# Kernel optimization log

Measured on AMD Instinct MI355X. Metric: run time of the kernel, lower is better.

Reference implementation:

```python
import jax, jax.numpy as jnp
import numpy as np


def squash(s, axis=-1):
    sq = jnp.sum(s * s, axis=axis, keepdims=True)
    return sq / (1.0 + sq) * s / (jnp.sqrt(sq) + 1e-8)


def setup_inputs() -> dict:
    key = jax.random.key(0)
    k1, k2 = jax.random.split(key)
    B, IN_CAPS, IN_DIM = 32, 2048, 16
    NUM_CAPS, CAPS_DIM = 32, 32
    x = jax.random.normal(k1, (B, IN_CAPS, IN_DIM), dtype=jnp.float32)
    W = 0.01 * jax.random.normal(k2, (NUM_CAPS, IN_CAPS, CAPS_DIM, IN_DIM), dtype=jnp.float32)
    return {"x": x, "W": W, "routing_steps": 3}


def reference(x, W, routing_steps):
    # u_hat[b, j, i, c] = W[j, i, c, d] @ x[b, i, d]
    u_hat = jnp.einsum('jicd,bid->bjic', W, x)
    du = jax.lax.stop_gradient(u_hat)  # routing uses detached predictions
    B, J, I, C = u_hat.shape
    b = jnp.zeros((B, J, I, 1), dtype=u_hat.dtype)
    for _ in range(routing_steps - 1):
        c = jax.nn.softmax(b, axis=1)                  # over output capsules j
        s = jnp.sum(c * du, axis=2)                    # [B, J, C]
        v = squash(s)
        b = b + jnp.einsum('bjic,bjc->bji', du, v)[..., None]
    c = jax.nn.softmax(b, axis=1)
    s = jnp.sum(c * u_hat, axis=2)
    v = squash(s)                                      # [B, J, C]
    return v
```

## Files before the change

### kernel.cpp

```cpp
#include <hip/hip_runtime.h>
#include <hip/hip_bf16.h>

#define B_SZ   32
#define I_CAPS 2048
#define J_CAPS 32
#define C_DIM  32
#define D_DIM  16

#define IT     8
#define TILES  8
#define SPLIT  32
#define ROW_STRIDE 40
#define MPAD   72

typedef _Float16 f16x8 __attribute__((ext_vector_type(8)));
typedef _Float16 f16x4 __attribute__((ext_vector_type(4)));
typedef float    f32x4 __attribute__((ext_vector_type(4)));

__device__ __forceinline__ float h2f_lo(unsigned int p) {
    union { unsigned short s; _Float16 h; } cv; cv.s = (unsigned short)(p & 0xffffu);
    return (float)cv.h;
}
__device__ __forceinline__ float h2f_hi(unsigned int p) { return h2f_lo(p >> 16); }

__global__ __launch_bounds__(256) void uhat_mfma(const float* __restrict__ W,
                                                 const float* __restrict__ x,
                                                 unsigned short* __restrict__ u) {
    const int t    = threadIdx.x;
    const int wave = t >> 6;
    const int lane = t & 63;
    const int lm   = lane & 15;
    const int lq   = lane >> 4;

    __shared__ unsigned short tr[4][32 * MPAD];
    unsigned short* my = tr[wave];

    const int i = blockIdx.x;

    f16x8 bfr[2];
#pragma unroll
    for (int nt = 0; nt < 2; ++nt) {
        const int b = nt * 16 + lm;
        const float4 xv = *reinterpret_cast<const float4*>(
            &x[((size_t)b * I_CAPS + i) * D_DIM + lq * 4]);
        f16x8 f = {};
        f[0] = (_Float16)xv.x; f[1] = (_Float16)xv.y;
        f[2] = (_Float16)xv.z; f[3] = (_Float16)xv.w;
        bfr[nt] = f;
    }

    float4 wv[16];
#pragma unroll
    for (int k = 0; k < 16; ++k) {
        const int mt = wave * 16 + k;
        const int j  = mt >> 1;
        const int c  = (mt & 1) * 16 + lm;
        wv[k] = *reinterpret_cast<const float4*>(
            &W[(((size_t)j * I_CAPS + i) * C_DIM + c) * D_DIM + lq * 4]);
    }

#pragma unroll
    for (int g = 0; g < 4; ++g) {
#pragma unroll
        for (int k4 = 0; k4 < 4; ++k4) {
            const int k = g * 4 + k4;
            f16x8 a = {};
            a[0] = (_Float16)wv[k].x; a[1] = (_Float16)wv[k].y;
            a[2] = (_Float16)wv[k].z; a[3] = (_Float16)wv[k].w;

            const f32x4 z = {0.f, 0.f, 0.f, 0.f};
            f32x4 d0 = __builtin_amdgcn_mfma_f32_16x16x32_f16(a, bfr[0], z, 0, 0, 0);
            f32x4 d1 = __builtin_amdgcn_mfma_f32_16x16x32_f16(a, bfr[1], z, 0, 0, 0);

            const int m_loc = k4 * 16 + lq * 4;
#pragma unroll
            for (int nt = 0; nt < 2; ++nt) {
                const f32x4 d = nt ? d1 : d0;
                f16x4 o;
                o[0] = (_Float16)d[0]; o[1] = (_Float16)d[1];
                o[2] = (_Float16)d[2]; o[3] = (_Float16)d[3];
                const int b = nt * 16 + lm;
                *reinterpret_cast<f16x4*>(&my[b * MPAD + m_loc]) = o;
            }
        }
        asm volatile("s_waitcnt lgkmcnt(0)" ::: "memory");
        __builtin_amdgcn_sched_barrier(0);

        const int b_off = lane >> 3;
        const int m_off = (lane & 7) * 8;
        const int m_base = wave * 256 + g * 64;
#pragma unroll
        for (int gb = 0; gb < 4; ++gb) {
            const int b = gb * 8 + b_off;
            const uint4 v = *reinterpret_cast<const uint4*>(&my[b * MPAD + m_off]);
            *reinterpret_cast<uint4*>(
                &u[((size_t)b * I_CAPS + i) * (J_CAPS * C_DIM) + m_base + m_off]) = v;
        }
    }
}

__global__ __launch_bounds__(256) void route_pass(const unsigned short* __restrict__ u,
                                                  const float* __restrict__ s_prev,
                                                  float* __restrict__ V1,
                                                  float* __restrict__ s_out,
                                                  int pass) {
    const int b      = blockIdx.y;
    const int isplit = blockIdx.x;
    const int i_base = isplit * (IT * TILES);
    const int t      = threadIdx.x;

    __shared__ unsigned short us[IT * J_CAPS * ROW_STRIDE];
    __shared__ float Vs[J_CAPS * 33];
    __shared__ float cjs[IT * J_CAPS];

    const int jA = t & 31, iA = t >> 5;
    const int jB = t >> 3, c4 = (t & 7) * 4;

    if (pass > 0) {
        const size_t base = ((size_t)b * J_CAPS + jB) * C_DIM + c4;
        const float4 sv = *reinterpret_cast<const float4*>(&s_prev[base]);
        float sq = sv.x * sv.x + sv.y * sv.y + sv.z * sv.z + sv.w * sv.w;
#pragma unroll
        for (int msk = 4; msk >= 1; msk >>= 1) sq += __shfl_xor(sq, msk);
        const float scale = sq / ((1.f + sq) * (sqrtf(sq) + 1e-8f));
        float4 v;
        v.x = sv.x * scale; v.y = sv.y * scale;
        v.z = sv.z * scale; v.w = sv.w * scale;
        if (pass == 1 && isplit == 0)
            *reinterpret_cast<float4*>(&V1[base]) = v;
        if (pass == 2) {
            const float4 v1 = *reinterpret_cast<const float4*>(&V1[base]);
            v.x += v1.x; v.y += v1.y; v.z += v1.z; v.w += v1.w;
        }
        Vs[jB * 33 + c4 + 0] = v.x; Vs[jB * 33 + c4 + 1] = v.y;
        Vs[jB * 33 + c4 + 2] = v.z; Vs[jB * 33 + c4 + 3] = v.w;
    }

    float sacc0 = 0.f, sacc1 = 0.f, sacc2 = 0.f, sacc3 = 0.f;

    const uint4* gbase = reinterpret_cast<const uint4*>(
        u + ((size_t)b * I_CAPS + i_base) * (J_CAPS * C_DIM));
#define TSRC(tile) (gbase + (size_t)(tile) * 1024)

    uint4 rA0, rA1, rA2, rA3, rB0, rB1, rB2, rB3;
    { const uint4* g = TSRC(0); rA0 = g[t]; rA1 = g[t+256]; rA2 = g[t+512]; rA3 = g[t+768]; }

#define STAGE_WRITE(R0, R1, R2, R3)                                             \
    {                                                                           \
        _Pragma("unroll")                                                       \
        for (int k = 0; k < 4; ++k) {                                           \
            const int n  = t + k * 256;                                         \
            const int il = n >> 7, rem = n & 127, j = rem >> 2, q = rem & 3;    \
            const uint4 rv = (k == 0) ? R0 : (k == 1) ? R1 : (k == 2) ? R2 : R3;\
            *reinterpret_cast<uint4*>(                                          \
                &us[(il * J_CAPS + j) * ROW_STRIDE + q * 8]) = rv;              \
        }                                                                       \
    }

#define PHASES(TILE_)                                                           \
    {                                                                           \
        __syncthreads();                                                        \
        if (pass == 0) {                                                        \
            cjs[iA * J_CAPS + jA] = 1.0f / 32.0f;                               \
        } else {                                                                \
            const unsigned short* row = &us[(iA * J_CAPS + jA) * ROW_STRIDE];   \
            float l = 0.f;                                                      \
            _Pragma("unroll")                                                   \
            for (int cq = 0; cq < 8; ++cq) {                                    \
                const uint2 pk = *reinterpret_cast<const uint2*>(row + cq * 4); \
                const float* Vr = &Vs[jA * 33 + cq * 4];                        \
                l += h2f_lo(pk.x) * Vr[0] + h2f_hi(pk.x) * Vr[1]                \
                   + h2f_lo(pk.y) * Vr[2] + h2f_hi(pk.y) * Vr[3];               \
            }                                                                   \
            float m = l;                                                        \
            _Pragma("unroll")                                                   \
            for (int msk = 16; msk >= 1; msk >>= 1) m = fmaxf(m, __shfl_xor(m, msk)); \
            const float e = __expf(l - m);                                      \
            float ssum = e;                                                     \
            _Pragma("unroll")                                                   \
            for (int msk = 16; msk >= 1; msk >>= 1) ssum += __shfl_xor(ssum, msk); \
            cjs[iA * J_CAPS + jA] = e / ssum;                                   \
        }                                                                       \
        __syncthreads();                                                        \
        _Pragma("unroll")                                                       \
        for (int il = 0; il < IT; ++il) {                                       \
            const float cj = cjs[il * J_CAPS + jB];                             \
            const unsigned short* row = &us[(il * J_CAPS + jB) * ROW_STRIDE + c4]; \
            const uint2 pk = *reinterpret_cast<const uint2*>(row);              \
            sacc0 += cj * h2f_lo(pk.x);                                         \
            sacc1 += cj * h2f_hi(pk.x);                                         \
            sacc2 += cj * h2f_lo(pk.y);                                         \
            sacc3 += cj * h2f_hi(pk.y);                                         \
        }                                                                       \
    }

#pragma unroll
    for (int tp = 0; tp < TILES / 2; ++tp) {
        __syncthreads();
        STAGE_WRITE(rA0, rA1, rA2, rA3);
        { const uint4* g = TSRC(2 * tp + 1); rB0 = g[t]; rB1 = g[t+256]; rB2 = g[t+512]; rB3 = g[t+768]; }
        PHASES(2 * tp)

        __syncthreads();
        STAGE_WRITE(rB0, rB1, rB2, rB3);
        if (tp + 1 < TILES / 2) {
            const uint4* g = TSRC(2 * tp + 2); rA0 = g[t]; rA1 = g[t+256]; rA2 = g[t+512]; rA3 = g[t+768];
        }
        PHASES(2 * tp + 1)
    }
#undef TSRC
#undef STAGE_WRITE
#undef PHASES

    float* sp = &s_out[((size_t)b * J_CAPS + jB) * C_DIM + c4];
    atomicAdd(sp + 0, sacc0);
    atomicAdd(sp + 1, sacc1);
    atomicAdd(sp + 2, sacc2);
    atomicAdd(sp + 3, sacc3);
}

__global__ __launch_bounds__(256) void squash_out(const float* __restrict__ s,
                                                  float* __restrict__ out) {
    const int t   = threadIdx.x;
    const int row = blockIdx.x * 8 + (t >> 5);
    const int c   = t & 31;
    const float sv = s[row * 32 + c];
    float sq = sv * sv;
#pragma unroll
    for (int msk = 16; msk >= 1; msk >>= 1) sq += __shfl_xor(sq, msk);
    const float scale = sq / ((1.f + sq) * (sqrtf(sq) + 1e-8f));
    out[row * 32 + c] = sv * scale;
}

extern "C" void kernel_launch(void* const* d_in, const int* in_sizes, int n_in,
                              void* d_out, int out_size, void* d_ws, size_t ws_size,
                              hipStream_t stream) {
    const float* x = (const float*)d_in[0];
    const float* W = (const float*)d_in[1];
    float* out = (float*)d_out;

    const size_t u_elems = (size_t)B_SZ * I_CAPS * J_CAPS * C_DIM;
    const size_t sjc     = (size_t)B_SZ * J_CAPS * C_DIM;

    unsigned short* u = (unsigned short*)d_ws;
    float* s0 = (float*)((char*)d_ws + u_elems * 2);
    float* s1 = s0 + sjc;
    float* s2 = s1 + sjc;
    float* V1 = s2 + sjc;

    hipMemsetAsync(s0, 0, 4 * sjc * sizeof(float), stream);

    uhat_mfma<<<I_CAPS, 256, 0, stream>>>(W, x, u);

    route_pass<<<dim3(SPLIT, B_SZ), 256, 0, stream>>>(u, nullptr, V1, s0, 0);
    route_pass<<<dim3(SPLIT, B_SZ), 256, 0, stream>>>(u, s0, V1, s1, 1);
    route_pass<<<dim3(SPLIT, B_SZ), 256, 0, stream>>>(u, s1, V1, s2, 2);

    squash_out<<<(B_SZ * J_CAPS * C_DIM) / 256, 256, 0, stream>>>(s2, out);
}
```

Measured before the change: 165.3 us.

## Double-buffer W and x tiles into LDS via async global_load_lds in u_hat kernel

The u_hat MFMA kernel now processes 8 input capsules per block instead of one. It stages each capsule's W slice and x slice into LDS with asynchronous global_load_lds copies and double-buffers them, so the next capsule's load overlaps the current one's MFMA work and u_hat stores. This is meant to hide global load latency and cut the per-block launch and setup cost. In exchange it uses about 150KB of dynamic LDS, which allows only one block (four waves) per CU and may reduce the latency hiding that occupancy used to provide.

```diff
diff --git a/kernel.cpp b/kernel.cpp
--- a/kernel.cpp
+++ b/kernel.cpp
@@ -13,6 +13,15 @@
 #define ROW_STRIDE 40
 #define MPAD   72
 
+#define IPB    8
+
+#define OFF_W0 0
+#define OFF_W1 65536
+#define OFF_X0 131072
+#define OFF_X1 133120
+#define OFF_TR 135168
+#define SMEM_BYTES 153600
+
 typedef _Float16 f16x8 __attribute__((ext_vector_type(8)));
 typedef _Float16 f16x4 __attribute__((ext_vector_type(4)));
 typedef float    f32x4 __attribute__((ext_vector_type(4)));
@@ -23,80 +32,114 @@
 }
 __device__ __forceinline__ float h2f_hi(unsigned int p) { return h2f_lo(p >> 16); }
 
+__device__ __forceinline__ void gl_lds16(const float* src, char* dst) {
+    __builtin_amdgcn_global_load_lds(
+        (const __attribute__((address_space(1))) void*)src,
+        (__attribute__((address_space(3))) void*)dst, 16, 0, 0);
+}
+
 __global__ __launch_bounds__(256) void uhat_mfma(const float* __restrict__ W,
                                                  const float* __restrict__ x,
                                                  unsigned short* __restrict__ u) {
+    extern __shared__ char smem[];
     const int t    = threadIdx.x;
     const int wave = t >> 6;
     const int lane = t & 63;
     const int lm   = lane & 15;
     const int lq   = lane >> 4;
 
-    __shared__ unsigned short tr[4][32 * MPAD];
-    unsigned short* my = tr[wave];
-
-    const int i = blockIdx.x;
-
-    f16x8 bfr[2];
-#pragma unroll
-    for (int nt = 0; nt < 2; ++nt) {
-        const int b = nt * 16 + lm;
-        const float4 xv = *reinterpret_cast<const float4*>(
-            &x[((size_t)b * I_CAPS + i) * D_DIM + lq * 4]);
-        f16x8 f = {};
-        f[0] = (_Float16)xv.x; f[1] = (_Float16)xv.y;
-        f[2] = (_Float16)xv.z; f[3] = (_Float16)xv.w;
-        bfr[nt] = f;
-    }
-
-    float4 wv[16];
-#pragma unroll
-    for (int k = 0; k < 16; ++k) {
-        const int mt = wave * 16 + k;
-        const int j  = mt >> 1;
-        const int c  = (mt & 1) * 16 + lm;
-        wv[k] = *reinterpret_cast<const float4*>(
-            &W[(((size_t)j * I_CAPS + i) * C_DIM + c) * D_DIM + lq * 4]);
-    }
-
-#pragma unroll
-    for (int g = 0; g < 4; ++g) {
-#pragma unroll
-        for (int k4 = 0; k4 < 4; ++k4) {
-            const int k = g * 4 + k4;
-            f16x8 a = {};
-            a[0] = (_Float16)wv[k].x; a[1] = (_Float16)wv[k].y;
-            a[2] = (_Float16)wv[k].z; a[3] = (_Float16)wv[k].w;
-
-            const f32x4 z = {0.f, 0.f, 0.f, 0.f};
-            f32x4 d0 = __builtin_amdgcn_mfma_f32_16x16x32_f16(a, bfr[0], z, 0, 0, 0);
-            f32x4 d1 = __builtin_amdgcn_mfma_f32_16x16x32_f16(a, bfr[1], z, 0, 0, 0);
-
-            const int m_loc = k4 * 16 + lq * 4;
-#pragma unroll
-            for (int nt = 0; nt < 2; ++nt) {
-                const f32x4 d = nt ? d1 : d0;
-                f16x4 o;
-                o[0] = (_Float16)d[0]; o[1] = (_Float16)d[1];
-                o[2] = (_Float16)d[2]; o[3] = (_Float16)d[3];
-                const int b = nt * 16 + lm;
-                *reinterpret_cast<f16x4*>(&my[b * MPAD + m_loc]) = o;
+    unsigned short* my = (unsigned short*)(smem + OFF_TR) + wave * (32 * MPAD);
+
+    const int i_first = blockIdx.x * IPB;
+
+#define STAGE(IDX, BF)                                                          \
+    {                                                                           \
+        char* wdst = smem + ((BF) ? OFF_W1 : OFF_W0);                           \
+        char* xdst = smem + ((BF) ? OFF_X1 : OFF_X0);                           \
+        _Pragma("unroll")                                                       \
+        for (int k = 0; k < 16; ++k) {                                          \
+            const int s = k * 256 + t;                                          \
+            const int m = s & 1023, q = s >> 10;                                \
+            const float* src = W + (size_t)(m >> 5) * (I_CAPS * C_DIM * D_DIM)  \
+                                 + (size_t)(IDX) * (C_DIM * D_DIM)              \
+                                 + (m & 31) * D_DIM + q * 4;                    \
+            gl_lds16(src, wdst + (size_t)s * 16);                               \
+        }                                                                       \
+        if (t < 128) {                                                          \
+            const int b = t & 31, q = t >> 5;                                   \
+            const float* src = x + ((size_t)b * I_CAPS + (IDX)) * D_DIM + q * 4;\
+            gl_lds16(src, xdst + (size_t)t * 16);                               \
+        }                                                                       \
+    }
+
+    STAGE(i_first, 0)
+    __syncthreads();
+
+    const int b_off = lane >> 3;
+    const int m_off = (lane & 7) * 8;
+
+    for (int ii = 0; ii < IPB; ++ii) {
+        const int i   = i_first + ii;
+        const int cur = ii & 1;
+
+        if (ii + 1 < IPB) STAGE(i_first + ii + 1, cur ^ 1)
+
+        const char* wbuf = smem + (cur ? OFF_W1 : OFF_W0);
+        const char* xbuf = smem + (cur ? OFF_X1 : OFF_X0);
+
+        f16x8 bfr0 = {}, bfr1 = {};
+        {
+            const float4 xv0 = *reinterpret_cast<const float4*>(
+                xbuf + (size_t)(lq * 32 + lm) * 16);
+            const float4 xv1 = *reinterpret_cast<const float4*>(
+                xbuf + (size_t)(lq * 32 + 16 + lm) * 16);
+            bfr0[0] = (_Float16)xv0.x; bfr0[1] = (_Float16)xv0.y;
+            bfr0[2] = (_Float16)xv0.z; bfr0[3] = (_Float16)xv0.w;
+            bfr1[0] = (_Float16)xv1.x; bfr1[1] = (_Float16)xv1.y;
+            bfr1[2] = (_Float16)xv1.z; bfr1[3] = (_Float16)xv1.w;
+        }
+
+#pragma unroll
+        for (int g = 0; g < 4; ++g) {
+#pragma unroll
+            for (int k4 = 0; k4 < 4; ++k4) {
+                const int mt = wave * 16 + g * 4 + k4;
+                const int m  = mt * 16 + lm;
+                const float4 wf = *reinterpret_cast<const float4*>(
+                    wbuf + (size_t)(lq * 1024 + m) * 16);
+                f16x8 a = {};
+                a[0] = (_Float16)wf.x; a[1] = (_Float16)wf.y;
+                a[2] = (_Float16)wf.z; a[3] = (_Float16)wf.w;
+
+                const f32x4 z = {0.f, 0.f, 0.f, 0.f};
+                f32x4 d0 = __builtin_amdgcn_mfma_f32_16x16x32_f16(a, bfr0, z, 0, 0, 0);
+                f32x4 d1 = __builtin_amdgcn_mfma_f32_16x16x32_f16(a, bfr1, z, 0, 0, 0);
+
+                const int m_loc = k4 * 16 + lq * 4;
+                f16x4 o0, o1;
+                o0[0] = (_Float16)d0[0]; o0[1] = (_Float16)d0[1];
+                o0[2] = (_Float16)d0[2]; o0[3] = (_Float16)d0[3];
+                o1[0] = (_Float16)d1[0]; o1[1] = (_Float16)d1[1];
+                o1[2] = (_Float16)d1[2]; o1[3] = (_Float16)d1[3];
+                *reinterpret_cast<f16x4*>(&my[lm * MPAD + m_loc])        = o0;
+                *reinterpret_cast<f16x4*>(&my[(16 + lm) * MPAD + m_loc]) = o1;
+            }
+            asm volatile("s_waitcnt lgkmcnt(0)" ::: "memory");
+            __builtin_amdgcn_sched_barrier(0);
+
+            const int m_base = wave * 256 + g * 64;
+#pragma unroll
+            for (int gb = 0; gb < 4; ++gb) {
+                const int b = gb * 8 + b_off;
+                const uint4 v = *reinterpret_cast<const uint4*>(&my[b * MPAD + m_off]);
+                *reinterpret_cast<uint4*>(
+                    &u[((size_t)b * I_CAPS + i) * (J_CAPS * C_DIM) + m_base + m_off]) = v;
             }
         }
-        asm volatile("s_waitcnt lgkmcnt(0)" ::: "memory");
-        __builtin_amdgcn_sched_barrier(0);
-
-        const int b_off = lane >> 3;
-        const int m_off = (lane & 7) * 8;
-        const int m_base = wave * 256 + g * 64;
-#pragma unroll
-        for (int gb = 0; gb < 4; ++gb) {
-            const int b = gb * 8 + b_off;
-            const uint4 v = *reinterpret_cast<const uint4*>(&my[b * MPAD + m_off]);
-            *reinterpret_cast<uint4*>(
-                &u[((size_t)b * I_CAPS + i) * (J_CAPS * C_DIM) + m_base + m_off]) = v;
-        }
-    }
+
+        __syncthreads();
+    }
+#undef STAGE
 }
 
 __global__ __launch_bounds__(256) void route_pass(const unsigned short* __restrict__ u,
@@ -248,9 +291,11 @@
     float* s2 = s1 + sjc;
     float* V1 = s2 + sjc;
 
-    hipMemsetAsync(s0, 0, 4 * sjc * sizeof(float), stream);
-
-    uhat_mfma<<<I_CAPS, 256, 0, stream>>>(W, x, u);
+    (void)hipMemsetAsync(s0, 0, 4 * sjc * sizeof(float), stream);
+
+    (void)hipFuncSetAttribute((const void*)uhat_mfma,
+                              hipFuncAttributeMaxDynamicSharedMemorySize, SMEM_BYTES);
+    uhat_mfma<<<I_CAPS / IPB, 256, SMEM_BYTES, stream>>>(W, x, u);
 
     route_pass<<<dim3(SPLIT, B_SZ), 256, 0, stream>>>(u, nullptr, V1, s0, 0);
     route_pass<<<dim3(SPLIT, B_SZ), 256, 0, stream>>>(u, s0, V1, s1, 1);
```

After: 172.5 us. 4.3% more time.
